# Kernel optimization log

Hardware: AMD Instinct MI355X
Metric: run time of the kernel (lower is better)

Reference implementation:

```python
import jax, jax.numpy as jnp
import numpy as np

# Dims: M=batch, T=time frames, B=bottleneck channels, H=intermediate channels, KK=kernel size
M, T, B, H, KK = 8, 4000, 128, 512, 3
DILATION = 2
EPS = 1e-8  # gLN eps (ConvTasNet convention)


def prelu(x, a):
    return jnp.where(x >= 0, x, a * x)


def gln(x, gamma, beta):
    # global layer norm over (time, channel) per sample; x: [M, T, C]
    m = jnp.mean(x, axis=(1, 2), keepdims=True)
    v = jnp.mean((x - m) ** 2, axis=(1, 2), keepdims=True)
    return gamma * (x - m) / jnp.sqrt(v + EPS) + beta


def depthwise_conv_same_reflect(x, w):
    # x: [M, C, L], w: [C, K]; dilation 1, 'same' padding with reflect mode
    K = w.shape[1]
    pl = (K - 1) // 2
    xp = jnp.pad(x, ((0, 0), (0, 0), (pl, K - 1 - pl)), mode='reflect')
    return jax.lax.conv_general_dilated(
        xp, w[:, None, :], (1,), 'VALID',
        feature_group_count=x.shape[1], dimension_numbers=('NCH', 'OIH', 'NCH'))


def setup_inputs() -> dict:
    key = jax.random.key(0)
    ks = jax.random.split(key, 12)
    f32 = jnp.float32
    return {
        'x': jax.random.normal(ks[0], (M, T, B), f32),
        'conv1_w': jax.random.normal(ks[1], (H, B), f32) * 0.05,
        'prelu1_a': jnp.asarray(0.25, f32),
        'norm1_g': jnp.ones((H,), f32),
        'norm1_b': jnp.zeros((H,), f32),
        'off_dw_w': jax.random.normal(ks[2], (H, KK), f32) * 0.02,
        'odc_prelu_a': jnp.asarray(0.25, f32),
        'off_pw_w': jax.random.normal(ks[3], (KK, H), f32) * 0.02,
        'opc_prelu_a': jnp.asarray(0.25, f32),
        'dw_w': jax.random.normal(ks[4], (H, KK), f32) * 0.05,
        'dw_b': jax.random.normal(ks[5], (H,), f32) * 0.01,
        'prelu2_a': jnp.asarray(0.25, f32),
        'norm2_g': jnp.ones((H,), f32),
        'norm2_b': jnp.zeros((H,), f32),
        'pw_w': jax.random.normal(ks[6], (B, H), f32) * 0.05,
    }


def reference(x, conv1_w, prelu1_a, norm1_g, norm1_b,
              off_dw_w, odc_prelu_a, off_pw_w, opc_prelu_a,
              dw_w, dw_b, prelu2_a, norm2_g, norm2_b, pw_w):
    dtype = x.dtype
    residual = x
    # 1x1 bottleneck conv -> PReLU -> gLN
    h = jnp.einsum('mtb,hb->mth', x, conv1_w)
    h = gln(prelu(h, prelu1_a), norm1_g, norm1_b)
    hc = jnp.moveaxis(h, 1, 2)  # [M, H, T]

    # --- offset prediction branch (PackedDeformConv1d) ---
    off = depthwise_conv_same_reflect(hc, off_dw_w)          # [M, H, T]
    off = prelu(off, odc_prelu_a)
    off = jnp.einsum('mct,kc->mkt', off, off_pw_w)           # [M, KK, T]
    off = prelu(off, opc_prelu_a)
    offsets = jnp.moveaxis(off, 1, 2)                        # [M, T, KK]

    # --- deformable depthwise conv (same padding, reflect) ---
    pad_tot = DILATION * (KK - 1)
    pl = pad_tot // 2
    xp = jnp.pad(hc, ((0, 0), (0, 0), (pl, pad_tot - pl)), mode='reflect')  # [M,H,Lp]
    Lp = T + pad_tot
    dil_pos = (jnp.arange(KK) * DILATION).astype(dtype)      # [KK]: 0, d, 2d
    t0 = jnp.arange(T, dtype=dtype)[:, None]                 # [T,1]
    Tpos = t0 + dil_pos[None, :] + offsets                   # [M,T,KK]
    Tpos = jnp.clip(Tpos, t0, t0 + dil_pos[-1])              # constrain to receptive field
    U = jnp.clip(jnp.floor(Tpos).astype(jnp.int32), 0, Lp - 2)
    Uf = U.astype(dtype)
    g0 = jax.nn.relu(1.0 - jnp.abs(Uf - Tpos))               # [M,T,KK]
    g1 = jax.nn.relu(1.0 - jnp.abs(Uf + 1.0 - Tpos))
    idx = jnp.broadcast_to(U.reshape(M, 1, T * KK), (M, H, T * KK))
    s0 = jnp.take_along_axis(xp, idx, axis=2).reshape(M, H, T, KK)
    s1 = jnp.take_along_axis(xp, idx + 1, axis=2).reshape(M, H, T, KK)
    sampled = g0[:, None] * s0 + g1[:, None] * s1            # [M,H,T,KK]
    y = jnp.einsum('mhtk,hk->mht', sampled, dw_w) + dw_b[None, :, None]

    # PReLU -> gLN -> 1x1 conv back to B channels, residual add
    y = jnp.moveaxis(y, 1, 2)                                # [M,T,H]
    y = gln(prelu(y, prelu2_a), norm2_g, norm2_b)
    out = jnp.einsum('mth,bh->mtb', y, pw_w)
    return out + residual
```

## Files before the change

kernel.cpp:

```cpp
#include <hip/hip_runtime.h>

#define Mdim 8
#define Tdim 4000
#define Bdim 128
#define Hdim 512
#define NPER (Tdim*Hdim)
#define EPSG 1e-8f

typedef __attribute__((ext_vector_type(8))) short short8;
typedef __attribute__((ext_vector_type(4))) float floatx4;

static __device__ __forceinline__ float bits2f(unsigned short s) {
  union { unsigned int u; float f; } v; v.u = ((unsigned int)s) << 16; return v.f;
}
static __device__ __forceinline__ unsigned short f2bits(float f) {
  union { float f; unsigned int u; } v; v.f = f;
  unsigned int u = v.u;
  u += 0x7fffu + ((u >> 16) & 1u);
  return (unsigned short)(u >> 16);
}
static __device__ __forceinline__ short8 pack8(const float4& a, const float4& b) {
  short8 v;
  v[0]=(short)f2bits(a.x); v[1]=(short)f2bits(a.y); v[2]=(short)f2bits(a.z); v[3]=(short)f2bits(a.w);
  v[4]=(short)f2bits(b.x); v[5]=(short)f2bits(b.y); v[6]=(short)f2bits(b.z); v[7]=(short)f2bits(b.w);
  return v;
}

__global__ __launch_bounds__(256) void k_conv1(
    const float* __restrict__ x,
    const float* __restrict__ w1,
    const float* __restrict__ a1p,
    unsigned short* __restrict__ Hbuf,
    float2* __restrict__ part1)
{
  __shared__ __align__(16) unsigned short ldsW[64*136];
  __shared__ __align__(16) unsigned short ltile[64*72];
  __shared__ float red[512];

  const int tid = threadIdx.x;
  const int t0 = blockIdx.x * 64;
  const int hh = blockIdx.y;
  const int m  = blockIdx.z;

  const int lane = tid & 63, wv = tid >> 6, quad = lane >> 4, l16 = lane & 15;
  int tr = t0 + wv*16 + l16;
  int trc = tr < Tdim ? tr : Tdim-1;
  const float* xrow = x + ((size_t)m*Tdim + trc)*Bdim;
  short8 afr[4];
  #pragma unroll
  for (int ks = 0; ks < 4; ++ks) {
    float4 fa = *(const float4*)&xrow[ks*32 + quad*8];
    float4 fb = *(const float4*)&xrow[ks*32 + quad*8 + 4];
    afr[ks] = pack8(fa, fb);
  }

  const float a1 = a1p[0];
  float lsum = 0.f, lss = 0.f;

  for (int hc = 0; hc < 4; ++hc) {
    const int h0 = (hh*4 + hc) * 64;
    __syncthreads();
    #pragma unroll
    for (int it = 0; it < 4; ++it) {
      int idx = (it*256 + tid) * 8;
      int r = idx >> 7, c = idx & 127;
      float4 fa = *(const float4*)&w1[(size_t)(h0 + r)*Bdim + c];
      float4 fb = *(const float4*)&w1[(size_t)(h0 + r)*Bdim + c + 4];
      *(short8*)&ldsW[r*136 + c] = pack8(fa, fb);
    }
    __syncthreads();

    floatx4 acc[4] = {};
    #pragma unroll
    for (int ks = 0; ks < 4; ++ks) {
      #pragma unroll
      for (int nt = 0; nt < 4; ++nt) {
        short8 bfr = *(const short8*)&ldsW[(nt*16 + l16)*136 + ks*32 + quad*8];
        acc[nt] = __builtin_amdgcn_mfma_f32_16x16x32_bf16(afr[ks], bfr, acc[nt], 0, 0, 0);
      }
    }

    #pragma unroll
    for (int nt = 0; nt < 4; ++nt) {
      int hl = nt*16 + l16;
      #pragma unroll
      for (int r = 0; r < 4; ++r) {
        int tl = wv*16 + quad*4 + r;
        float v = acc[nt][r];
        v = v >= 0.f ? v : a1 * v;
        if (t0 + tl < Tdim) { lsum += v; lss += v*v; }
        ltile[tl*72 + hl] = f2bits(v);
      }
    }
    __syncthreads();
    {
      int tr2 = tid >> 2, ck = (tid & 3) * 16;
      int tg = t0 + tr2;
      if (tg < Tdim) {
        unsigned short* dst = &Hbuf[((size_t)m*Tdim + tg)*Hdim + h0 + ck];
        *(short8*)&dst[0] = *(const short8*)&ltile[tr2*72 + ck];
        *(short8*)&dst[8] = *(const short8*)&ltile[tr2*72 + ck + 8];
      }
    }
  }

  red[tid] = lsum; red[256 + tid] = lss;
  __syncthreads();
  for (int s = 128; s > 0; s >>= 1) {
    if (tid < s) { red[tid] += red[tid + s]; red[256+tid] += red[256+tid+s]; }
    __syncthreads();
  }
  if (tid == 0)
    part1[((size_t)m*2 + hh)*63 + blockIdx.x] = make_float2(red[0], red[256]);
}

__global__ __launch_bounds__(256) void k_deform(
    const unsigned short* __restrict__ Hbuf,
    const float2* __restrict__ part1,
    const float* __restrict__ g1w,
    const float* __restrict__ b1w,
    const float* __restrict__ odw,
    const float* __restrict__ aodcp,
    const float* __restrict__ opw,
    const float* __restrict__ aopcp,
    const float* __restrict__ dww,
    const float* __restrict__ dwb,
    const float* __restrict__ a2p,
    unsigned short* __restrict__ Ybuf,
    float2* __restrict__ part2)
{
  __shared__ float s_stats[2];
  __shared__ float rsum[4], rss[4];
  const int tid = threadIdx.x, lane = tid & 63, w = tid >> 6;
  const int tb = blockIdx.x*8 + w*2;
  const int m = blockIdx.y;
  const int c8 = lane*8;
  const unsigned short* base = Hbuf + (size_t)m*Tdim*Hdim;

  short8 hrow[2][3];
  #pragma unroll
  for (int tt = 0; tt < 2; ++tt) {
    int t = tb + tt;
    int tm1 = (t == 0) ? 1 : t-1;
    int tp1 = (t == Tdim-1) ? Tdim-2 : t+1;
    hrow[tt][0] = *(const short8*)&base[(size_t)tm1*Hdim + c8];
    hrow[tt][1] = *(const short8*)&base[(size_t)t  *Hdim + c8];
    hrow[tt][2] = *(const short8*)&base[(size_t)tp1*Hdim + c8];
  }
  float g1v[8], b1v[8];
  #pragma unroll
  for (int j = 0; j < 8; j += 4) {
    *(float4*)&g1v[j] = *(const float4*)&g1w[c8 + j];
    *(float4*)&b1v[j] = *(const float4*)&b1w[c8 + j];
  }

  if (tid < 64) {
    float s = 0.f, q = 0.f;
    for (int i = lane; i < 126; i += 64) {
      float2 p = part1[(size_t)m*126 + i];
      s += p.x; q += p.y;
    }
    #pragma unroll
    for (int st = 32; st > 0; st >>= 1) { s += __shfl_xor(s, st); q += __shfl_xor(q, st); }
    if (lane == 0) { s_stats[0] = s; s_stats[1] = q; }
  }
  __syncthreads();
  const float invn = 1.0f/(float)NPER;
  const float mean1 = s_stats[0]*invn;
  const float var1  = fmaxf(s_stats[1]*invn - mean1*mean1, 0.f);
  const float inv1  = 1.0f/sqrtf(var1 + EPSG);

  float oa[2][3] = {};
  {
    const float aodc = aodcp[0];
    float wod[24], q0v[8], q1v[8], q2v[8];
    #pragma unroll
    for (int j = 0; j < 8; j += 4) {
      *(float4*)&q0v[j] = *(const float4*)&opw[c8 + j];
      *(float4*)&q1v[j] = *(const float4*)&opw[Hdim + c8 + j];
      *(float4*)&q2v[j] = *(const float4*)&opw[2*Hdim + c8 + j];
    }
    #pragma unroll
    for (int j = 0; j < 24; j += 4)
      *(float4*)&wod[j] = *(const float4*)&odw[c8*3 + j];

    #pragma unroll
    for (int j = 0; j < 8; ++j) {
      float A = g1v[j] * inv1;
      float C = b1v[j] - mean1*A;
      #pragma unroll
      for (int tt = 0; tt < 2; ++tt) {
        float fm = fmaf(A, bits2f((unsigned short)hrow[tt][0][j]), C);
        float fz = fmaf(A, bits2f((unsigned short)hrow[tt][1][j]), C);
        float fp = fmaf(A, bits2f((unsigned short)hrow[tt][2][j]), C);
        float d = fm*wod[j*3+0] + fz*wod[j*3+1] + fp*wod[j*3+2];
        d = d >= 0.f ? d : aodc*d;
        oa[tt][0] = fmaf(d, q0v[j], oa[tt][0]);
        oa[tt][1] = fmaf(d, q1v[j], oa[tt][1]);
        oa[tt][2] = fmaf(d, q2v[j], oa[tt][2]);
      }
    }
    #pragma unroll
    for (int s = 32; s > 0; s >>= 1) {
      #pragma unroll
      for (int tt = 0; tt < 2; ++tt) {
        oa[tt][0] += __shfl_xor(oa[tt][0], s);
        oa[tt][1] += __shfl_xor(oa[tt][1], s);
        oa[tt][2] += __shfl_xor(oa[tt][2], s);
      }
    }
  }

  const float aopc = aopcp[0];
  const float a2   = a2p[0];
  int I0[2][3], I1[2][3]; float G0[2][3], G1[2][3], GS[2][3];
  #pragma unroll
  for (int tt = 0; tt < 2; ++tt) {
    const float tf = (float)(tb + tt);
    #pragma unroll
    for (int k = 0; k < 3; ++k) {
      float off = oa[tt][k];
      off = off >= 0.f ? off : aopc*off;
      float pos = tf + (float)(2*k) + off;
      pos = fminf(fmaxf(pos, tf), tf + 4.0f);
      int U = (int)floorf(pos);
      if (U > Tdim + 2) U = Tdim + 2;
      float Uf = (float)U;
      G0[tt][k] = fmaxf(0.f, 1.f - fabsf(Uf - pos));
      G1[tt][k] = fmaxf(0.f, 1.f - fabsf(Uf + 1.f - pos));
      GS[tt][k] = G0[tt][k] + G1[tt][k];
      int ia = U - 2; ia = ia < 0 ? -ia : ia; if (ia > Tdim-1) ia = 2*(Tdim-1) - ia;
      int ib = U - 1; ib = ib < 0 ? -ib : ib; if (ib > Tdim-1) ib = 2*(Tdim-1) - ib;
      I0[tt][k] = ia; I1[tt][k] = ib;
    }
  }

  short8 s0v[2][3], s1v[2][3];
  #pragma unroll
  for (int tt = 0; tt < 2; ++tt)
    #pragma unroll
    for (int k = 0; k < 3; ++k) {
      s0v[tt][k] = *(const short8*)&base[(size_t)I0[tt][k]*Hdim + c8];
      s1v[tt][k] = *(const short8*)&base[(size_t)I1[tt][k]*Hdim + c8];
    }

  float bv[8], wd[24];
  #pragma unroll
  for (int j = 0; j < 8; j += 4)
    *(float4*)&bv[j] = *(const float4*)&dwb[c8 + j];
  #pragma unroll
  for (int j = 0; j < 24; j += 4)
    *(float4*)&wd[j] = *(const float4*)&dww[c8*3 + j];

  float lsum = 0.f, lss = 0.f;
  short8 yv[2];
  #pragma unroll
  for (int j = 0; j < 8; ++j) {
    float A = g1v[j] * inv1;
    float C = b1v[j] - mean1*A;
    float w0 = wd[j*3+0], w1 = wd[j*3+1], w2 = wd[j*3+2];
    #pragma unroll
    for (int tt = 0; tt < 2; ++tt) {
      float ybase = fmaf(C, w0*GS[tt][0] + w1*GS[tt][1] + w2*GS[tt][2], bv[j]);
      float t0s = fmaf(G1[tt][0], bits2f((unsigned short)s1v[tt][0][j]), G0[tt][0]*bits2f((unsigned short)s0v[tt][0][j]));
      float t1s = fmaf(G1[tt][1], bits2f((unsigned short)s1v[tt][1][j]), G0[tt][1]*bits2f((unsigned short)s0v[tt][1][j]));
      float t2s = fmaf(G1[tt][2], bits2f((unsigned short)s1v[tt][2][j]), G0[tt][2]*bits2f((unsigned short)s0v[tt][2][j]));
      float acc = w0*t0s + w1*t1s + w2*t2s;
      float y = fmaf(A, acc, ybase);
      float p = y >= 0.f ? y : a2*y;
      lsum += p; lss += p*p;
      yv[tt][j] = (short)f2bits(p);
    }
  }
  #pragma unroll
  for (int tt = 0; tt < 2; ++tt)
    *(short8*)&Ybuf[((size_t)m*Tdim + tb + tt)*Hdim + c8] = yv[tt];

  #pragma unroll
  for (int s = 32; s > 0; s >>= 1) {
    lsum += __shfl_xor(lsum, s);
    lss  += __shfl_xor(lss, s);
  }
  if (lane == 0) { rsum[w] = lsum; rss[w] = lss; }
  __syncthreads();
  if (tid == 0)
    part2[(size_t)m*500 + blockIdx.x] =
      make_float2(rsum[0]+rsum[1]+rsum[2]+rsum[3], rss[0]+rss[1]+rss[2]+rss[3]);
}

__global__ __launch_bounds__(64) void k_w2(
    const float2* __restrict__ part2,
    const float* __restrict__ g2w,
    const float* __restrict__ b2w,
    const float* __restrict__ pww,
    unsigned short* __restrict__ W2,
    float* __restrict__ const2)
{
  const int bid = blockIdx.x;
  const int m = bid >> 7, b = bid & 127;
  const int tid = threadIdx.x;

  float s = 0.f, q = 0.f;
  for (int i = tid; i < 500; i += 64) {
    float2 p = part2[(size_t)m*500 + i];
    s += p.x; q += p.y;
  }
  #pragma unroll
  for (int st = 32; st > 0; st >>= 1) { s += __shfl_xor(s, st); q += __shfl_xor(q, st); }

  const float invn = 1.0f/(float)NPER;
  const float mean2 = s*invn;
  const float var2  = fmaxf(q*invn - mean2*mean2, 0.f);
  const float inv2  = 1.0f/sqrtf(var2 + EPSG);

  const int j8 = tid*8;
  float g2v[8], b2v[8], pv[8];
  #pragma unroll
  for (int j = 0; j < 8; j += 4) {
    *(float4*)&g2v[j] = *(const float4*)&g2w[j8 + j];
    *(float4*)&b2v[j] = *(const float4*)&b2w[j8 + j];
    *(float4*)&pv[j]  = *(const float4*)&pww[(size_t)b*Hdim + j8 + j];
  }
  float csum = 0.f;
  short8 wv8;
  #pragma unroll
  for (int j = 0; j < 8; ++j) {
    float A = g2v[j] * inv2;
    float C = b2v[j] - mean2*A;
    csum = fmaf(C, pv[j], csum);
    wv8[j] = (short)f2bits(A*pv[j]);
  }
  *(short8*)&W2[((size_t)m*Bdim + b)*Hdim + j8] = wv8;

  #pragma unroll
  for (int st = 32; st > 0; st >>= 1) csum += __shfl_down(csum, st);
  if (tid == 0) const2[m*Bdim + b] = csum;
}

__global__ __launch_bounds__(256) void k_out(
    const unsigned short* __restrict__ Ybuf,
    const unsigned short* __restrict__ W2,
    const float* __restrict__ const2,
    const float* __restrict__ x,
    float* __restrict__ out)
{
  __shared__ __align__(16) unsigned short ldsW[64*136];
  __shared__ __align__(16) float ltf[64*68];
  const int tid = threadIdx.x;
  const int t0 = blockIdx.x*64;
  const int n0 = blockIdx.y*64;
  const int m  = blockIdx.z;
  const int lane = tid & 63, wv = tid >> 6, quad = lane >> 4, l16 = lane & 15;
  int tr = t0 + wv*16 + l16;
  int trc = tr < Tdim ? tr : Tdim-1;
  const unsigned short* arow = Ybuf + ((size_t)m*Tdim + trc)*Hdim;
  floatx4 acc[4] = {};
  for (int kc = 0; kc < 4; ++kc) {
    __syncthreads();
    #pragma unroll
    for (int it = 0; it < 4; ++it) {
      int idx = (it*256 + tid)*8;
      int r = idx >> 7, c = idx & 127;
      *(short8*)&ldsW[r*136 + c] =
        *(const short8*)&W2[((size_t)m*Bdim + n0 + r)*Hdim + kc*128 + c];
    }
    __syncthreads();
    #pragma unroll
    for (int ks = 0; ks < 4; ++ks) {
      short8 afr = *(const short8*)&arow[kc*128 + ks*32 + quad*8];
      #pragma unroll
      for (int nt = 0; nt < 4; ++nt) {
        short8 bfr = *(const short8*)&ldsW[(nt*16 + l16)*136 + ks*32 + quad*8];
        acc[nt] = __builtin_amdgcn_mfma_f32_16x16x32_bf16(afr, bfr, acc[nt], 0, 0, 0);
      }
    }
  }
  __syncthreads();
  #pragma unroll
  for (int nt = 0; nt < 4; ++nt) {
    int bl = nt*16 + l16;
    float cb = const2[m*Bdim + n0 + bl];
    #pragma unroll
    for (int r = 0; r < 4; ++r) {
      int tl = wv*16 + quad*4 + r;
      ltf[tl*68 + bl] = acc[nt][r] + cb;
    }
  }
  __syncthreads();
  {
    int tr2 = tid >> 2, ck = (tid & 3) * 16;
    int tg = t0 + tr2;
    if (tg < Tdim) {
      const float* xr = &x[((size_t)m*Tdim + tg)*Bdim + n0 + ck];
      float* orow = &out[((size_t)m*Tdim + tg)*Bdim + n0 + ck];
      #pragma unroll
      for (int j = 0; j < 4; ++j) {
        float4 v = *(const float4*)&ltf[tr2*68 + ck + j*4];
        float4 rx = *(const float4*)&xr[j*4];
        v.x += rx.x; v.y += rx.y; v.z += rx.z; v.w += rx.w;
        *(float4*)&orow[j*4] = v;
      }
    }
  }
}

extern "C" void kernel_launch(void* const* d_in, const int* in_sizes, int n_in,
                              void* d_out, int out_size, void* d_ws, size_t ws_size,
                              hipStream_t stream)
{
  (void)in_sizes; (void)n_in; (void)out_size; (void)ws_size;
  const float* x    = (const float*)d_in[0];
  const float* w1   = (const float*)d_in[1];
  const float* a1   = (const float*)d_in[2];
  const float* g1   = (const float*)d_in[3];
  const float* b1   = (const float*)d_in[4];
  const float* odw  = (const float*)d_in[5];
  const float* aodc = (const float*)d_in[6];
  const float* opw  = (const float*)d_in[7];
  const float* aopc = (const float*)d_in[8];
  const float* dww  = (const float*)d_in[9];
  const float* dwb  = (const float*)d_in[10];
  const float* a2   = (const float*)d_in[11];
  const float* g2   = (const float*)d_in[12];
  const float* b2   = (const float*)d_in[13];
  const float* pww  = (const float*)d_in[14];
  float* out = (float*)d_out;

  char* ws = (char*)d_ws;
  const size_t OFF_P1 = 0;
  const size_t OFF_C2 = 8192;
  const size_t OFF_P2 = 12288;
  const size_t OFF_W2 = 44288;
  const size_t OFF_H  = 1092864;
  const size_t OFF_Y  = 33860864;
  float2* part1  = (float2*)(ws + OFF_P1);
  float*  const2 = (float*)(ws + OFF_C2);
  float2* part2  = (float2*)(ws + OFF_P2);
  unsigned short* W2   = (unsigned short*)(ws + OFF_W2);
  unsigned short* Hbuf = (unsigned short*)(ws + OFF_H);
  unsigned short* Ybuf = (unsigned short*)(ws + OFF_Y);

  k_conv1 <<<dim3(63, 2, 8), 256, 0, stream>>>(x, w1, a1, Hbuf, part1);
  k_deform<<<dim3(500, 8), 256, 0, stream>>>(Hbuf, part1, g1, b1, odw, aodc, opw, aopc, dww, dwb, a2, Ybuf, part2);
  k_w2    <<<dim3(1024), 64, 0, stream>>>(part2, g2, b2, pww, W2, const2);
  k_out   <<<dim3(63, 2, 8), 256, 0, stream>>>(Ybuf, W2, const2, x, out);
}
```

Before: 165.6 us.

## Stage H time tile in LDS for deform gather and pre-swizzle GEMM weights

```diff
diff --git a/kernel.cpp b/kernel.cpp
--- a/kernel.cpp
+++ b/kernel.cpp
@@ -6,6 +6,7 @@
 #define Hdim 512
 #define NPER (Tdim*Hdim)
 #define EPSG 1e-8f
+#define ROWS 69
 
 typedef __attribute__((ext_vector_type(8))) short short8;
 typedef __attribute__((ext_vector_type(4))) float floatx4;
@@ -26,22 +27,38 @@
   return v;
 }
 
+#define LDS_FENCE() do { \
+  asm volatile("s_waitcnt lgkmcnt(0)" ::: "memory"); \
+  __builtin_amdgcn_sched_barrier(0); \
+} while (0)
+
+__global__ __launch_bounds__(256) void k_prep(
+    const float* __restrict__ w1, unsigned short* __restrict__ w1r)
+{
+  int i = blockIdx.x*256 + threadIdx.x;
+  int lane = i & 63, f = i >> 6;
+  int nt = f & 3, ks = (f >> 2) & 3, hc = f >> 4;
+  int h = hc*64 + nt*16 + (lane & 15);
+  int c = ks*32 + (lane >> 4)*8;
+  const float* src = &w1[(size_t)h*Bdim + c];
+  float4 a = *(const float4*)src;
+  float4 b = *(const float4*)(src + 4);
+  *(short8*)&w1r[(size_t)i*8] = pack8(a, b);
+}
+
 __global__ __launch_bounds__(256) void k_conv1(
     const float* __restrict__ x,
-    const float* __restrict__ w1,
+    const unsigned short* __restrict__ w1r,
     const float* __restrict__ a1p,
     unsigned short* __restrict__ Hbuf,
     float2* __restrict__ part1)
 {
-  __shared__ __align__(16) unsigned short ldsW[64*136];
   __shared__ __align__(16) unsigned short ltile[64*72];
   __shared__ float red[512];
 
   const int tid = threadIdx.x;
   const int t0 = blockIdx.x * 64;
-  const int hh = blockIdx.y;
-  const int m  = blockIdx.z;
-
+  const int m  = blockIdx.y;
   const int lane = tid & 63, wv = tid >> 6, quad = lane >> 4, l16 = lane & 15;
   int tr = t0 + wv*16 + l16;
   int trc = tr < Tdim ? tr : Tdim-1;
@@ -55,30 +72,17 @@
   }
 
   const float a1 = a1p[0];
+  const short8* wf = (const short8*)w1r + lane;
   float lsum = 0.f, lss = 0.f;
 
-  for (int hc = 0; hc < 4; ++hc) {
-    const int h0 = (hh*4 + hc) * 64;
-    __syncthreads();
-    #pragma unroll
-    for (int it = 0; it < 4; ++it) {
-      int idx = (it*256 + tid) * 8;
-      int r = idx >> 7, c = idx & 127;
-      float4 fa = *(const float4*)&w1[(size_t)(h0 + r)*Bdim + c];
-      float4 fb = *(const float4*)&w1[(size_t)(h0 + r)*Bdim + c + 4];
-      *(short8*)&ldsW[r*136 + c] = pack8(fa, fb);
-    }
-    __syncthreads();
-
+  for (int hc = 0; hc < 8; ++hc) {
     floatx4 acc[4] = {};
     #pragma unroll
-    for (int ks = 0; ks < 4; ++ks) {
-      #pragma unroll
-      for (int nt = 0; nt < 4; ++nt) {
-        short8 bfr = *(const short8*)&ldsW[(nt*16 + l16)*136 + ks*32 + quad*8];
-        acc[nt] = __builtin_amdgcn_mfma_f32_16x16x32_bf16(afr[ks], bfr, acc[nt], 0, 0, 0);
-      }
-    }
+    for (int ks = 0; ks < 4; ++ks)
+      #pragma unroll
+      for (int nt = 0; nt < 4; ++nt)
+        acc[nt] = __builtin_amdgcn_mfma_f32_16x16x32_bf16(
+            afr[ks], wf[(hc*16 + ks*4 + nt)*64], acc[nt], 0, 0, 0);
 
     #pragma unroll
     for (int nt = 0; nt < 4; ++nt) {
@@ -92,16 +96,17 @@
         ltile[tl*72 + hl] = f2bits(v);
       }
     }
-    __syncthreads();
+    LDS_FENCE();
     {
       int tr2 = tid >> 2, ck = (tid & 3) * 16;
       int tg = t0 + tr2;
       if (tg < Tdim) {
-        unsigned short* dst = &Hbuf[((size_t)m*Tdim + tg)*Hdim + h0 + ck];
+        unsigned short* dst = &Hbuf[((size_t)m*Tdim + tg)*Hdim + hc*64 + ck];
         *(short8*)&dst[0] = *(const short8*)&ltile[tr2*72 + ck];
         *(short8*)&dst[8] = *(const short8*)&ltile[tr2*72 + ck + 8];
       }
     }
+    LDS_FENCE();
   }
 
   red[tid] = lsum; red[256 + tid] = lss;
@@ -111,7 +116,7 @@
     __syncthreads();
   }
   if (tid == 0)
-    part1[((size_t)m*2 + hh)*63 + blockIdx.x] = make_float2(red[0], red[256]);
+    part1[(size_t)m*63 + blockIdx.x] = make_float2(red[0], red[256]);
 }
 
 __global__ __launch_bounds__(256) void k_deform(
@@ -129,65 +134,88 @@
     unsigned short* __restrict__ Ybuf,
     float2* __restrict__ part2)
 {
+  __shared__ __align__(16) unsigned short tile[ROWS*512];
   __shared__ float s_stats[2];
   __shared__ float rsum[4], rss[4];
   const int tid = threadIdx.x, lane = tid & 63, w = tid >> 6;
-  const int tb = blockIdx.x*8 + w*2;
+  const int t0 = blockIdx.x * 64;
   const int m = blockIdx.y;
   const int c8 = lane*8;
   const unsigned short* base = Hbuf + (size_t)m*Tdim*Hdim;
 
-  short8 hrow[2][3];
-  #pragma unroll
-  for (int tt = 0; tt < 2; ++tt) {
-    int t = tb + tt;
-    int tm1 = (t == 0) ? 1 : t-1;
-    int tp1 = (t == Tdim-1) ? Tdim-2 : t+1;
-    hrow[tt][0] = *(const short8*)&base[(size_t)tm1*Hdim + c8];
-    hrow[tt][1] = *(const short8*)&base[(size_t)t  *Hdim + c8];
-    hrow[tt][2] = *(const short8*)&base[(size_t)tp1*Hdim + c8];
-  }
-  float g1v[8], b1v[8];
-  #pragma unroll
-  for (int j = 0; j < 8; j += 4) {
-    *(float4*)&g1v[j] = *(const float4*)&g1w[c8 + j];
-    *(float4*)&b1v[j] = *(const float4*)&b1w[c8 + j];
+  short8 stg[17];
+  #pragma unroll
+  for (int i = 0; i < 17; ++i) {
+    int s = t0 - 2 + w + i*4;
+    s = s < 0 ? -s : s;
+    if (s > Tdim-1) s = 2*(Tdim-1) - s;
+    stg[i] = *(const short8*)&base[(size_t)s*Hdim + c8];
+  }
+  short8 extra;
+  if (w == 0) {
+    int s = t0 + 66;
+    if (s > Tdim-1) s = 2*(Tdim-1) - s;
+    extra = *(const short8*)&base[(size_t)s*Hdim + c8];
   }
 
   if (tid < 64) {
     float s = 0.f, q = 0.f;
-    for (int i = lane; i < 126; i += 64) {
-      float2 p = part1[(size_t)m*126 + i];
-      s += p.x; q += p.y;
-    }
+    if (lane < 63) { float2 p = part1[(size_t)m*63 + lane]; s = p.x; q = p.y; }
     #pragma unroll
     for (int st = 32; st > 0; st >>= 1) { s += __shfl_xor(s, st); q += __shfl_xor(q, st); }
     if (lane == 0) { s_stats[0] = s; s_stats[1] = q; }
   }
+
+  #pragma unroll
+  for (int i = 0; i < 17; ++i)
+    *(short8*)&tile[(w + i*4)*512 + c8] = stg[i];
+  if (w == 0) *(short8*)&tile[68*512 + c8] = extra;
+
   __syncthreads();
+
   const float invn = 1.0f/(float)NPER;
   const float mean1 = s_stats[0]*invn;
   const float var1  = fmaxf(s_stats[1]*invn - mean1*mean1, 0.f);
   const float inv1  = 1.0f/sqrtf(var1 + EPSG);
 
-  float oa[2][3] = {};
-  {
-    const float aodc = aodcp[0];
-    float wod[24], q0v[8], q1v[8], q2v[8];
-    #pragma unroll
-    for (int j = 0; j < 8; j += 4) {
-      *(float4*)&q0v[j] = *(const float4*)&opw[c8 + j];
-      *(float4*)&q1v[j] = *(const float4*)&opw[Hdim + c8 + j];
-      *(float4*)&q2v[j] = *(const float4*)&opw[2*Hdim + c8 + j];
-    }
-    #pragma unroll
-    for (int j = 0; j < 24; j += 4)
-      *(float4*)&wod[j] = *(const float4*)&odw[c8*3 + j];
-
+  const float aodc = aodcp[0], aopc = aopcp[0], a2 = a2p[0];
+  float wod[24], q0v[8], q1v[8], q2v[8], wd[24], bv[8], Ax[8], Cx[8];
+  #pragma unroll
+  for (int j = 0; j < 8; j += 4) {
+    *(float4*)&q0v[j] = *(const float4*)&opw[c8 + j];
+    *(float4*)&q1v[j] = *(const float4*)&opw[Hdim + c8 + j];
+    *(float4*)&q2v[j] = *(const float4*)&opw[2*Hdim + c8 + j];
+    *(float4*)&bv[j]  = *(const float4*)&dwb[c8 + j];
+  }
+  #pragma unroll
+  for (int j = 0; j < 24; j += 4) {
+    *(float4*)&wod[j] = *(const float4*)&odw[c8*3 + j];
+    *(float4*)&wd[j]  = *(const float4*)&dww[c8*3 + j];
+  }
+  #pragma unroll
+  for (int j = 0; j < 8; ++j) {
+    Ax[j] = g1w[c8 + j] * inv1;
+    Cx[j] = b1w[c8 + j] - mean1*Ax[j];
+  }
+
+  float lsum = 0.f, lss = 0.f;
+  #pragma unroll 1
+  for (int it = 0; it < 16; it += 2) {
+    const int t = t0 + w*16 + it;
+    if (t >= Tdim) break;
+    const int sb = t - t0 + 2;
+
+    short8 hrow[2][3];
+    #pragma unroll
+    for (int tt = 0; tt < 2; ++tt)
+      #pragma unroll
+      for (int k = 0; k < 3; ++k)
+        hrow[tt][k] = *(const short8*)&tile[(sb + tt - 1 + k)*512 + c8];
+
+    float oa[2][3] = {};
     #pragma unroll
     for (int j = 0; j < 8; ++j) {
-      float A = g1v[j] * inv1;
-      float C = b1v[j] - mean1*A;
+      float A = Ax[j], C = Cx[j];
       #pragma unroll
       for (int tt = 0; tt < 2; ++tt) {
         float fm = fmaf(A, bits2f((unsigned short)hrow[tt][0][j]), C);
@@ -201,90 +229,77 @@
       }
     }
     #pragma unroll
-    for (int s = 32; s > 0; s >>= 1) {
+    for (int st = 32; st > 0; st >>= 1) {
       #pragma unroll
       for (int tt = 0; tt < 2; ++tt) {
-        oa[tt][0] += __shfl_xor(oa[tt][0], s);
-        oa[tt][1] += __shfl_xor(oa[tt][1], s);
-        oa[tt][2] += __shfl_xor(oa[tt][2], s);
-      }
-    }
-  }
-
-  const float aopc = aopcp[0];
-  const float a2   = a2p[0];
-  int I0[2][3], I1[2][3]; float G0[2][3], G1[2][3], GS[2][3];
-  #pragma unroll
-  for (int tt = 0; tt < 2; ++tt) {
-    const float tf = (float)(tb + tt);
-    #pragma unroll
-    for (int k = 0; k < 3; ++k) {
-      float off = oa[tt][k];
-      off = off >= 0.f ? off : aopc*off;
-      float pos = tf + (float)(2*k) + off;
-      pos = fminf(fmaxf(pos, tf), tf + 4.0f);
-      int U = (int)floorf(pos);
-      if (U > Tdim + 2) U = Tdim + 2;
-      float Uf = (float)U;
-      G0[tt][k] = fmaxf(0.f, 1.f - fabsf(Uf - pos));
-      G1[tt][k] = fmaxf(0.f, 1.f - fabsf(Uf + 1.f - pos));
-      GS[tt][k] = G0[tt][k] + G1[tt][k];
-      int ia = U - 2; ia = ia < 0 ? -ia : ia; if (ia > Tdim-1) ia = 2*(Tdim-1) - ia;
-      int ib = U - 1; ib = ib < 0 ? -ib : ib; if (ib > Tdim-1) ib = 2*(Tdim-1) - ib;
-      I0[tt][k] = ia; I1[tt][k] = ib;
-    }
-  }
-
-  short8 s0v[2][3], s1v[2][3];
-  #pragma unroll
-  for (int tt = 0; tt < 2; ++tt)
-    #pragma unroll
-    for (int k = 0; k < 3; ++k) {
-      s0v[tt][k] = *(const short8*)&base[(size_t)I0[tt][k]*Hdim + c8];
-      s1v[tt][k] = *(const short8*)&base[(size_t)I1[tt][k]*Hdim + c8];
-    }
-
-  float bv[8], wd[24];
-  #pragma unroll
-  for (int j = 0; j < 8; j += 4)
-    *(float4*)&bv[j] = *(const float4*)&dwb[c8 + j];
-  #pragma unroll
-  for (int j = 0; j < 24; j += 4)
-    *(float4*)&wd[j] = *(const float4*)&dww[c8*3 + j];
-
-  float lsum = 0.f, lss = 0.f;
-  short8 yv[2];
-  #pragma unroll
-  for (int j = 0; j < 8; ++j) {
-    float A = g1v[j] * inv1;
-    float C = b1v[j] - mean1*A;
-    float w0 = wd[j*3+0], w1 = wd[j*3+1], w2 = wd[j*3+2];
+        oa[tt][0] += __shfl_xor(oa[tt][0], st);
+        oa[tt][1] += __shfl_xor(oa[tt][1], st);
+        oa[tt][2] += __shfl_xor(oa[tt][2], st);
+      }
+    }
+
+    int S0[2][3], S1[2][3]; float G0[2][3], G1[2][3], GS[2][3];
     #pragma unroll
     for (int tt = 0; tt < 2; ++tt) {
-      float ybase = fmaf(C, w0*GS[tt][0] + w1*GS[tt][1] + w2*GS[tt][2], bv[j]);
-      float t0s = fmaf(G1[tt][0], bits2f((unsigned short)s1v[tt][0][j]), G0[tt][0]*bits2f((unsigned short)s0v[tt][0][j]));
-      float t1s = fmaf(G1[tt][1], bits2f((unsigned short)s1v[tt][1][j]), G0[tt][1]*bits2f((unsigned short)s0v[tt][1][j]));
-      float t2s = fmaf(G1[tt][2], bits2f((unsigned short)s1v[tt][2][j]), G0[tt][2]*bits2f((unsigned short)s0v[tt][2][j]));
-      float acc = w0*t0s + w1*t1s + w2*t2s;
-      float y = fmaf(A, acc, ybase);
-      float p = y >= 0.f ? y : a2*y;
-      lsum += p; lss += p*p;
-      yv[tt][j] = (short)f2bits(p);
-    }
-  }
-  #pragma unroll
-  for (int tt = 0; tt < 2; ++tt)
-    *(short8*)&Ybuf[((size_t)m*Tdim + tb + tt)*Hdim + c8] = yv[tt];
-
-  #pragma unroll
-  for (int s = 32; s > 0; s >>= 1) {
-    lsum += __shfl_xor(lsum, s);
-    lss  += __shfl_xor(lss, s);
+      const float tf = (float)(t + tt);
+      #pragma unroll
+      for (int k = 0; k < 3; ++k) {
+        float off = oa[tt][k];
+        off = off >= 0.f ? off : aopc*off;
+        float pos = tf + (float)(2*k) + off;
+        pos = fminf(fmaxf(pos, tf), tf + 4.0f);
+        int U = (int)floorf(pos);
+        if (U > Tdim + 2) U = Tdim + 2;
+        float Uf = (float)U;
+        G0[tt][k] = fmaxf(0.f, 1.f - fabsf(Uf - pos));
+        G1[tt][k] = fmaxf(0.f, 1.f - fabsf(Uf + 1.f - pos));
+        GS[tt][k] = G0[tt][k] + G1[tt][k];
+        S0[tt][k] = U - t0;
+        S1[tt][k] = U - t0 + 1;
+      }
+    }
+
+    short8 s0v[2][3], s1v[2][3];
+    #pragma unroll
+    for (int tt = 0; tt < 2; ++tt)
+      #pragma unroll
+      for (int k = 0; k < 3; ++k) {
+        s0v[tt][k] = *(const short8*)&tile[S0[tt][k]*512 + c8];
+        s1v[tt][k] = *(const short8*)&tile[S1[tt][k]*512 + c8];
+      }
+
+    short8 yv[2];
+    #pragma unroll
+    for (int j = 0; j < 8; ++j) {
+      float A = Ax[j], C = Cx[j];
+      float w0 = wd[j*3+0], w1 = wd[j*3+1], w2 = wd[j*3+2];
+      #pragma unroll
+      for (int tt = 0; tt < 2; ++tt) {
+        float ybase = fmaf(C, w0*GS[tt][0] + w1*GS[tt][1] + w2*GS[tt][2], bv[j]);
+        float t0s = fmaf(G1[tt][0], bits2f((unsigned short)s1v[tt][0][j]), G0[tt][0]*bits2f((unsigned short)s0v[tt][0][j]));
+        float t1s = fmaf(G1[tt][1], bits2f((unsigned short)s1v[tt][1][j]), G0[tt][1]*bits2f((unsigned short)s0v[tt][1][j]));
+        float t2s = fmaf(G1[tt][2], bits2f((unsigned short)s1v[tt][2][j]), G0[tt][2]*bits2f((unsigned short)s0v[tt][2][j]));
+        float acc2 = w0*t0s + w1*t1s + w2*t2s;
+        float y = fmaf(A, acc2, ybase);
+        float p = y >= 0.f ? y : a2*y;
+        lsum += p; lss += p*p;
+        yv[tt][j] = (short)f2bits(p);
+      }
+    }
+    #pragma unroll
+    for (int tt = 0; tt < 2; ++tt)
+      *(short8*)&Ybuf[((size_t)m*Tdim + t + tt)*Hdim + c8] = yv[tt];
+  }
+
+  #pragma unroll
+  for (int st = 32; st > 0; st >>= 1) {
+    lsum += __shfl_xor(lsum, st);
+    lss  += __shfl_xor(lss, st);
   }
   if (lane == 0) { rsum[w] = lsum; rss[w] = lss; }
   __syncthreads();
   if (tid == 0)
-    part2[(size_t)m*500 + blockIdx.x] =
+    part2[(size_t)m*63 + blockIdx.x] =
       make_float2(rsum[0]+rsum[1]+rsum[2]+rsum[3], rss[0]+rss[1]+rss[2]+rss[3]);
 }
 
@@ -293,7 +308,7 @@
     const float* __restrict__ g2w,
     const float* __restrict__ b2w,
     const float* __restrict__ pww,
-    unsigned short* __restrict__ W2,
+    unsigned short* __restrict__ W2r,
     float* __restrict__ const2)
 {
   const int bid = blockIdx.x;
@@ -301,10 +316,7 @@
   const int tid = threadIdx.x;
 
   float s = 0.f, q = 0.f;
-  for (int i = tid; i < 500; i += 64) {
-    float2 p = part2[(size_t)m*500 + i];
-    s += p.x; q += p.y;
-  }
+  if (tid < 63) { float2 p = part2[(size_t)m*63 + tid]; s = p.x; q = p.y; }
   #pragma unroll
   for (int st = 32; st > 0; st >>= 1) { s += __shfl_xor(s, st); q += __shfl_xor(q, st); }
 
@@ -330,7 +342,13 @@
     csum = fmaf(C, pv[j], csum);
     wv8[j] = (short)f2bits(A*pv[j]);
   }
-  *(short8*)&W2[((size_t)m*Bdim + b)*Hdim + j8] = wv8;
+  {
+    int half = b >> 6, nt = (b >> 4) & 3, l16 = b & 15;
+    int kc = tid >> 4, ks = (tid >> 2) & 3, quad = tid & 3;
+    int lane = quad*16 + l16;
+    size_t f = ((((size_t)(m*2 + half)*4 + kc)*4 + ks)*4 + nt);
+    *(short8*)&W2r[(f*64 + lane)*8] = wv8;
+  }
 
   #pragma unroll
   for (int st = 32; st > 0; st >>= 1) csum += __shfl_down(csum, st);
@@ -339,43 +357,35 @@
 
 __global__ __launch_bounds__(256) void k_out(
     const unsigned short* __restrict__ Ybuf,
-    const unsigned short* __restrict__ W2,
+    const unsigned short* __restrict__ W2r,
     const float* __restrict__ const2,
     const float* __restrict__ x,
     float* __restrict__ out)
 {
-  __shared__ __align__(16) unsigned short ldsW[64*136];
   __shared__ __align__(16) float ltf[64*68];
   const int tid = threadIdx.x;
   const int t0 = blockIdx.x*64;
-  const int n0 = blockIdx.y*64;
+  const int half = blockIdx.y;
+  const int n0 = half*64;
   const int m  = blockIdx.z;
   const int lane = tid & 63, wv = tid >> 6, quad = lane >> 4, l16 = lane & 15;
   int tr = t0 + wv*16 + l16;
   int trc = tr < Tdim ? tr : Tdim-1;
   const unsigned short* arow = Ybuf + ((size_t)m*Tdim + trc)*Hdim;
+  const short8* wf = (const short8*)W2r + (size_t)(m*2 + half)*64*64 + lane;
+
   floatx4 acc[4] = {};
-  for (int kc = 0; kc < 4; ++kc) {
-    __syncthreads();
-    #pragma unroll
-    for (int it = 0; it < 4; ++it) {
-      int idx = (it*256 + tid)*8;
-      int r = idx >> 7, c = idx & 127;
-      *(short8*)&ldsW[r*136 + c] =
-        *(const short8*)&W2[((size_t)m*Bdim + n0 + r)*Hdim + kc*128 + c];
-    }
-    __syncthreads();
+  #pragma unroll
+  for (int kc = 0; kc < 4; ++kc)
     #pragma unroll
     for (int ks = 0; ks < 4; ++ks) {
       short8 afr = *(const short8*)&arow[kc*128 + ks*32 + quad*8];
       #pragma unroll
-      for (int nt = 0; nt < 4; ++nt) {
-        short8 bfr = *(const short8*)&ldsW[(nt*16 + l16)*136 + ks*32 + quad*8];
-        acc[nt] = __builtin_amdgcn_mfma_f32_16x16x32_bf16(afr, bfr, acc[nt], 0, 0, 0);
-      }
-    }
-  }
-  __syncthreads();
+      for (int nt = 0; nt < 4; ++nt)
+        acc[nt] = __builtin_amdgcn_mfma_f32_16x16x32_bf16(
+            afr, wf[((kc*4 + ks)*4 + nt)*64], acc[nt], 0, 0, 0);
+    }
+
   #pragma unroll
   for (int nt = 0; nt < 4; ++nt) {
     int bl = nt*16 + l16;
@@ -386,7 +396,7 @@
       ltf[tl*68 + bl] = acc[nt][r] + cb;
     }
   }
-  __syncthreads();
+  LDS_FENCE();
   {
     int tr2 = tid >> 2, ck = (tid & 3) * 16;
     int tg = t0 + tr2;
@@ -427,21 +437,24 @@
   float* out = (float*)d_out;
 
   char* ws = (char*)d_ws;
-  const size_t OFF_P1 = 0;
-  const size_t OFF_C2 = 8192;
-  const size_t OFF_P2 = 12288;
-  const size_t OFF_W2 = 44288;
-  const size_t OFF_H  = 1092864;
-  const size_t OFF_Y  = 33860864;
+  const size_t OFF_P1  = 0;
+  const size_t OFF_C2  = 4096;
+  const size_t OFF_P2  = 8192;
+  const size_t OFF_W1R = 12288;
+  const size_t OFF_W2  = 143360;
+  const size_t OFF_H   = 1191936;
+  const size_t OFF_Y   = 33959936;
   float2* part1  = (float2*)(ws + OFF_P1);
   float*  const2 = (float*)(ws + OFF_C2);
   float2* part2  = (float2*)(ws + OFF_P2);
-  unsigned short* W2   = (unsigned short*)(ws + OFF_W2);
+  unsigned short* w1r  = (unsigned short*)(ws + OFF_W1R);
+  unsigned short* W2r  = (unsigned short*)(ws + OFF_W2);
   unsigned short* Hbuf = (unsigned short*)(ws + OFF_H);
   unsigned short* Ybuf = (unsigned short*)(ws + OFF_Y);
 
-  k_conv1 <<<dim3(63, 2, 8), 256, 0, stream>>>(x, w1, a1, Hbuf, part1);
-  k_deform<<<dim3(500, 8), 256, 0, stream>>>(Hbuf, part1, g1, b1, odw, aodc, opw, aopc, dww, dwb, a2, Ybuf, part2);
-  k_w2    <<<dim3(1024), 64, 0, stream>>>(part2, g2, b2, pww, W2, const2);
-  k_out   <<<dim3(63, 2, 8), 256, 0, stream>>>(Ybuf, W2, const2, x, out);
-}
+  k_prep  <<<dim3(32), 256, 0, stream>>>(w1, w1r);
+  k_conv1 <<<dim3(63, 8), 256, 0, stream>>>(x, w1r, a1, Hbuf, part1);
+  k_deform<<<dim3(63, 8), 256, 0, stream>>>(Hbuf, part1, g1, b1, odw, aodc, opw, aopc, dww, dwb, a2, Ybuf, part2);
+  k_w2    <<<dim3(1024), 64, 0, stream>>>(part2, g2, b2, pww, W2r, const2);
+  k_out   <<<dim3(63, 2, 8), 256, 0, stream>>>(Ybuf, W2r, const2, x, out);
+}
```

After: 169.9 us. 2.6% more time.

## Fuse four kernels into one cooperative persistent kernel with grid syncs

Applied to the files above, without the earlier changes.

```diff
diff --git a/kernel.cpp b/kernel.cpp
--- a/kernel.cpp
+++ b/kernel.cpp
@@ -1,4 +1,5 @@
 #include <hip/hip_runtime.h>
+#include <hip/hip_cooperative_groups.h>
 
 #define Mdim 8
 #define Tdim 4000
@@ -26,26 +27,36 @@
   return v;
 }
 
-__global__ __launch_bounds__(256) void k_conv1(
-    const float* __restrict__ x,
-    const float* __restrict__ w1,
-    const float* __restrict__ a1p,
-    unsigned short* __restrict__ Hbuf,
-    float2* __restrict__ part1)
-{
-  __shared__ __align__(16) unsigned short ldsW[64*136];
-  __shared__ __align__(16) unsigned short ltile[64*72];
-  __shared__ float red[512];
+#define LDS_FENCE() do { \
+  asm volatile("s_waitcnt lgkmcnt(0)" ::: "memory"); \
+  __builtin_amdgcn_sched_barrier(0); \
+} while (0)
+
+struct P {
+  const float *x, *w1, *a1, *g1, *b1, *odw, *aodc, *opw, *aopc, *dww, *dwb, *a2, *g2, *b2, *pww;
+  float2 *part1, *part2;
+  float *const2;
+  unsigned short *W2r, *Hbuf, *Ybuf;
+  float *out;
+};
+
+#define SMEM_BYTES 28672
+
+__device__ __forceinline__ void phase_conv1(const P& p, int task, char* smem) {
+  unsigned short* ldsW  = (unsigned short*)smem;
+  unsigned short* ltile = (unsigned short*)(smem + 17408);
+  float* red = (float*)(smem + 26624);
 
   const int tid = threadIdx.x;
-  const int t0 = blockIdx.x * 64;
-  const int hh = blockIdx.y;
-  const int m  = blockIdx.z;
-
+  const int tile = task % 63;
+  const int rem  = task / 63;
+  const int hh = rem & 1;
+  const int m  = rem >> 1;
+  const int t0 = tile * 64;
   const int lane = tid & 63, wv = tid >> 6, quad = lane >> 4, l16 = lane & 15;
   int tr = t0 + wv*16 + l16;
   int trc = tr < Tdim ? tr : Tdim-1;
-  const float* xrow = x + ((size_t)m*Tdim + trc)*Bdim;
+  const float* xrow = p.x + ((size_t)m*Tdim + trc)*Bdim;
   short8 afr[4];
   #pragma unroll
   for (int ks = 0; ks < 4; ++ks) {
@@ -53,8 +64,7 @@
     float4 fb = *(const float4*)&xrow[ks*32 + quad*8 + 4];
     afr[ks] = pack8(fa, fb);
   }
-
-  const float a1 = a1p[0];
+  const float a1 = p.a1[0];
   float lsum = 0.f, lss = 0.f;
 
   for (int hc = 0; hc < 4; ++hc) {
@@ -64,8 +74,8 @@
     for (int it = 0; it < 4; ++it) {
       int idx = (it*256 + tid) * 8;
       int r = idx >> 7, c = idx & 127;
-      float4 fa = *(const float4*)&w1[(size_t)(h0 + r)*Bdim + c];
-      float4 fb = *(const float4*)&w1[(size_t)(h0 + r)*Bdim + c + 4];
+      float4 fa = *(const float4*)&p.w1[(size_t)(h0 + r)*Bdim + c];
+      float4 fb = *(const float4*)&p.w1[(size_t)(h0 + r)*Bdim + c + 4];
       *(short8*)&ldsW[r*136 + c] = pack8(fa, fb);
     }
     __syncthreads();
@@ -97,7 +107,7 @@
       int tr2 = tid >> 2, ck = (tid & 3) * 16;
       int tg = t0 + tr2;
       if (tg < Tdim) {
-        unsigned short* dst = &Hbuf[((size_t)m*Tdim + tg)*Hdim + h0 + ck];
+        unsigned short* dst = &p.Hbuf[((size_t)m*Tdim + tg)*Hdim + h0 + ck];
         *(short8*)&dst[0] = *(const short8*)&ltile[tr2*72 + ck];
         *(short8*)&dst[8] = *(const short8*)&ltile[tr2*72 + ck + 8];
       }
@@ -111,31 +121,22 @@
     __syncthreads();
   }
   if (tid == 0)
-    part1[((size_t)m*2 + hh)*63 + blockIdx.x] = make_float2(red[0], red[256]);
-}
-
-__global__ __launch_bounds__(256) void k_deform(
-    const unsigned short* __restrict__ Hbuf,
-    const float2* __restrict__ part1,
-    const float* __restrict__ g1w,
-    const float* __restrict__ b1w,
-    const float* __restrict__ odw,
-    const float* __restrict__ aodcp,
-    const float* __restrict__ opw,
-    const float* __restrict__ aopcp,
-    const float* __restrict__ dww,
-    const float* __restrict__ dwb,
-    const float* __restrict__ a2p,
-    unsigned short* __restrict__ Ybuf,
-    float2* __restrict__ part2)
-{
-  __shared__ float s_stats[2];
-  __shared__ float rsum[4], rss[4];
+    p.part1[((size_t)m*2 + hh)*63 + tile] = make_float2(red[0], red[256]);
+  __syncthreads();
+}
+
+__device__ __forceinline__ void phase_deform(const P& p, int task, char* smem) {
+  float* s_stats = (float*)smem;
+  float* rsum = (float*)smem + 2;
+  float* rss  = (float*)smem + 6;
   const int tid = threadIdx.x, lane = tid & 63, w = tid >> 6;
-  const int tb = blockIdx.x*8 + w*2;
-  const int m = blockIdx.y;
+  const int tx = task % 500;
+  const int m  = task / 500;
+  const int tb = tx*8 + w*2;
   const int c8 = lane*8;
-  const unsigned short* base = Hbuf + (size_t)m*Tdim*Hdim;
+  const unsigned short* base = p.Hbuf + (size_t)m*Tdim*Hdim;
+
+  __syncthreads();
 
   short8 hrow[2][3];
   #pragma unroll
@@ -150,15 +151,15 @@
   float g1v[8], b1v[8];
   #pragma unroll
   for (int j = 0; j < 8; j += 4) {
-    *(float4*)&g1v[j] = *(const float4*)&g1w[c8 + j];
-    *(float4*)&b1v[j] = *(const float4*)&b1w[c8 + j];
+    *(float4*)&g1v[j] = *(const float4*)&p.g1[c8 + j];
+    *(float4*)&b1v[j] = *(const float4*)&p.b1[c8 + j];
   }
 
   if (tid < 64) {
     float s = 0.f, q = 0.f;
     for (int i = lane; i < 126; i += 64) {
-      float2 p = part1[(size_t)m*126 + i];
-      s += p.x; q += p.y;
+      float2 pp = p.part1[(size_t)m*126 + i];
+      s += pp.x; q += pp.y;
     }
     #pragma unroll
     for (int st = 32; st > 0; st >>= 1) { s += __shfl_xor(s, st); q += __shfl_xor(q, st); }
@@ -172,17 +173,17 @@
 
   float oa[2][3] = {};
   {
-    const float aodc = aodcp[0];
+    const float aodc = p.aodc[0];
     float wod[24], q0v[8], q1v[8], q2v[8];
     #pragma unroll
     for (int j = 0; j < 8; j += 4) {
-      *(float4*)&q0v[j] = *(const float4*)&opw[c8 + j];
-      *(float4*)&q1v[j] = *(const float4*)&opw[Hdim + c8 + j];
-      *(float4*)&q2v[j] = *(const float4*)&opw[2*Hdim + c8 + j];
+      *(float4*)&q0v[j] = *(const float4*)&p.opw[c8 + j];
+      *(float4*)&q1v[j] = *(const float4*)&p.opw[Hdim + c8 + j];
+      *(float4*)&q2v[j] = *(const float4*)&p.opw[2*Hdim + c8 + j];
     }
     #pragma unroll
     for (int j = 0; j < 24; j += 4)
-      *(float4*)&wod[j] = *(const float4*)&odw[c8*3 + j];
+      *(float4*)&wod[j] = *(const float4*)&p.odw[c8*3 + j];
 
     #pragma unroll
     for (int j = 0; j < 8; ++j) {
@@ -211,8 +212,8 @@
     }
   }
 
-  const float aopc = aopcp[0];
-  const float a2   = a2p[0];
+  const float aopc = p.aopc[0];
+  const float a2   = p.a2[0];
   int I0[2][3], I1[2][3]; float G0[2][3], G1[2][3], GS[2][3];
   #pragma unroll
   for (int tt = 0; tt < 2; ++tt) {
@@ -247,10 +248,10 @@
   float bv[8], wd[24];
   #pragma unroll
   for (int j = 0; j < 8; j += 4)
-    *(float4*)&bv[j] = *(const float4*)&dwb[c8 + j];
+    *(float4*)&bv[j] = *(const float4*)&p.dwb[c8 + j];
   #pragma unroll
   for (int j = 0; j < 24; j += 4)
-    *(float4*)&wd[j] = *(const float4*)&dww[c8*3 + j];
+    *(float4*)&wd[j] = *(const float4*)&p.dww[c8*3 + j];
 
   float lsum = 0.f, lss = 0.f;
   short8 yv[2];
@@ -267,14 +268,14 @@
       float t2s = fmaf(G1[tt][2], bits2f((unsigned short)s1v[tt][2][j]), G0[tt][2]*bits2f((unsigned short)s0v[tt][2][j]));
       float acc = w0*t0s + w1*t1s + w2*t2s;
       float y = fmaf(A, acc, ybase);
-      float p = y >= 0.f ? y : a2*y;
-      lsum += p; lss += p*p;
-      yv[tt][j] = (short)f2bits(p);
+      float pp = y >= 0.f ? y : a2*y;
+      lsum += pp; lss += pp*pp;
+      yv[tt][j] = (short)f2bits(pp);
     }
   }
   #pragma unroll
   for (int tt = 0; tt < 2; ++tt)
-    *(short8*)&Ybuf[((size_t)m*Tdim + tb + tt)*Hdim + c8] = yv[tt];
+    *(short8*)&p.Ybuf[((size_t)m*Tdim + tb + tt)*Hdim + c8] = yv[tt];
 
   #pragma unroll
   for (int s = 32; s > 0; s >>= 1) {
@@ -284,26 +285,19 @@
   if (lane == 0) { rsum[w] = lsum; rss[w] = lss; }
   __syncthreads();
   if (tid == 0)
-    part2[(size_t)m*500 + blockIdx.x] =
+    p.part2[(size_t)m*500 + tx] =
       make_float2(rsum[0]+rsum[1]+rsum[2]+rsum[3], rss[0]+rss[1]+rss[2]+rss[3]);
 }
 
-__global__ __launch_bounds__(64) void k_w2(
-    const float2* __restrict__ part2,
-    const float* __restrict__ g2w,
-    const float* __restrict__ b2w,
-    const float* __restrict__ pww,
-    unsigned short* __restrict__ W2,
-    float* __restrict__ const2)
-{
-  const int bid = blockIdx.x;
-  const int m = bid >> 7, b = bid & 127;
+__device__ __forceinline__ void phase_w2(const P& p, int task) {
   const int tid = threadIdx.x;
+  if (tid >= 64) return;
+  const int m = task >> 7, b = task & 127;
 
   float s = 0.f, q = 0.f;
   for (int i = tid; i < 500; i += 64) {
-    float2 p = part2[(size_t)m*500 + i];
-    s += p.x; q += p.y;
+    float2 pp = p.part2[(size_t)m*500 + i];
+    s += pp.x; q += pp.y;
   }
   #pragma unroll
   for (int st = 32; st > 0; st >>= 1) { s += __shfl_xor(s, st); q += __shfl_xor(q, st); }
@@ -317,9 +311,9 @@
   float g2v[8], b2v[8], pv[8];
   #pragma unroll
   for (int j = 0; j < 8; j += 4) {
-    *(float4*)&g2v[j] = *(const float4*)&g2w[j8 + j];
-    *(float4*)&b2v[j] = *(const float4*)&b2w[j8 + j];
-    *(float4*)&pv[j]  = *(const float4*)&pww[(size_t)b*Hdim + j8 + j];
+    *(float4*)&g2v[j] = *(const float4*)&p.g2[j8 + j];
+    *(float4*)&b2v[j] = *(const float4*)&p.b2[j8 + j];
+    *(float4*)&pv[j]  = *(const float4*)&p.pww[(size_t)b*Hdim + j8 + j];
   }
   float csum = 0.f;
   short8 wv8;
@@ -330,69 +324,63 @@
     csum = fmaf(C, pv[j], csum);
     wv8[j] = (short)f2bits(A*pv[j]);
   }
-  *(short8*)&W2[((size_t)m*Bdim + b)*Hdim + j8] = wv8;
+  {
+    int half = b >> 6, nt = (b >> 4) & 3, l16 = b & 15;
+    int kc = tid >> 4, ks = (tid >> 2) & 3, quad = tid & 3;
+    int lane = quad*16 + l16;
+    size_t f = ((((size_t)(m*2 + half)*4 + kc)*4 + ks)*4 + nt);
+    *(short8*)&p.W2r[(f*64 + lane)*8] = wv8;
+  }
 
   #pragma unroll
   for (int st = 32; st > 0; st >>= 1) csum += __shfl_down(csum, st);
-  if (tid == 0) const2[m*Bdim + b] = csum;
-}
-
-__global__ __launch_bounds__(256) void k_out(
-    const unsigned short* __restrict__ Ybuf,
-    const unsigned short* __restrict__ W2,
-    const float* __restrict__ const2,
-    const float* __restrict__ x,
-    float* __restrict__ out)
-{
-  __shared__ __align__(16) unsigned short ldsW[64*136];
-  __shared__ __align__(16) float ltf[64*68];
+  if (tid == 0) p.const2[m*Bdim + b] = csum;
+}
+
+__device__ __forceinline__ void phase_out(const P& p, int task, char* smem) {
+  float* ltf = (float*)smem;
   const int tid = threadIdx.x;
-  const int t0 = blockIdx.x*64;
-  const int n0 = blockIdx.y*64;
-  const int m  = blockIdx.z;
+  const int tile = task % 63;
+  const int rem = task / 63;
+  const int half = rem & 1;
+  const int m = rem >> 1;
+  const int t0 = tile*64;
+  const int n0 = half*64;
   const int lane = tid & 63, wv = tid >> 6, quad = lane >> 4, l16 = lane & 15;
   int tr = t0 + wv*16 + l16;
   int trc = tr < Tdim ? tr : Tdim-1;
-  const unsigned short* arow = Ybuf + ((size_t)m*Tdim + trc)*Hdim;
+  const unsigned short* arow = p.Ybuf + ((size_t)m*Tdim + trc)*Hdim;
+  const short8* wf = (const short8*)p.W2r + (size_t)(m*2 + half)*64*64 + lane;
+
   floatx4 acc[4] = {};
-  for (int kc = 0; kc < 4; ++kc) {
-    __syncthreads();
-    #pragma unroll
-    for (int it = 0; it < 4; ++it) {
-      int idx = (it*256 + tid)*8;
-      int r = idx >> 7, c = idx & 127;
-      *(short8*)&ldsW[r*136 + c] =
-        *(const short8*)&W2[((size_t)m*Bdim + n0 + r)*Hdim + kc*128 + c];
-    }
-    __syncthreads();
+  #pragma unroll
+  for (int kc = 0; kc < 4; ++kc)
     #pragma unroll
     for (int ks = 0; ks < 4; ++ks) {
       short8 afr = *(const short8*)&arow[kc*128 + ks*32 + quad*8];
       #pragma unroll
-      for (int nt = 0; nt < 4; ++nt) {
-        short8 bfr = *(const short8*)&ldsW[(nt*16 + l16)*136 + ks*32 + quad*8];
-        acc[nt] = __builtin_amdgcn_mfma_f32_16x16x32_bf16(afr, bfr, acc[nt], 0, 0, 0);
-      }
-    }
-  }
-  __syncthreads();
+      for (int nt = 0; nt < 4; ++nt)
+        acc[nt] = __builtin_amdgcn_mfma_f32_16x16x32_bf16(
+            afr, wf[((kc*4 + ks)*4 + nt)*64], acc[nt], 0, 0, 0);
+    }
+
   #pragma unroll
   for (int nt = 0; nt < 4; ++nt) {
     int bl = nt*16 + l16;
-    float cb = const2[m*Bdim + n0 + bl];
+    float cb = p.const2[m*Bdim + n0 + bl];
     #pragma unroll
     for (int r = 0; r < 4; ++r) {
       int tl = wv*16 + quad*4 + r;
       ltf[tl*68 + bl] = acc[nt][r] + cb;
     }
   }
-  __syncthreads();
+  LDS_FENCE();
   {
     int tr2 = tid >> 2, ck = (tid & 3) * 16;
     int tg = t0 + tr2;
     if (tg < Tdim) {
-      const float* xr = &x[((size_t)m*Tdim + tg)*Bdim + n0 + ck];
-      float* orow = &out[((size_t)m*Tdim + tg)*Bdim + n0 + ck];
+      const float* xr = &p.x[((size_t)m*Tdim + tg)*Bdim + n0 + ck];
+      float* orow = &p.out[((size_t)m*Tdim + tg)*Bdim + n0 + ck];
       #pragma unroll
       for (int j = 0; j < 4; ++j) {
         float4 v = *(const float4*)&ltf[tr2*68 + ck + j*4];
@@ -402,6 +390,39 @@
       }
     }
   }
+  LDS_FENCE();
+}
+
+__global__ __launch_bounds__(256, 4) void k_fused(P p) {
+  __shared__ __align__(16) char smem[SMEM_BYTES];
+  cooperative_groups::grid_group g = cooperative_groups::this_grid();
+
+  for (int t = blockIdx.x; t < 1008; t += gridDim.x) phase_conv1(p, t, smem);
+  __threadfence();
+  g.sync();
+  for (int t = blockIdx.x; t < 4000; t += gridDim.x) phase_deform(p, t, smem);
+  __threadfence();
+  g.sync();
+  for (int t = blockIdx.x; t < 1024; t += gridDim.x) phase_w2(p, t);
+  __threadfence();
+  g.sync();
+  for (int t = blockIdx.x; t < 1008; t += gridDim.x) phase_out(p, t, smem);
+}
+
+__global__ __launch_bounds__(256, 4) void k_p1(P p) {
+  __shared__ __align__(16) char smem[SMEM_BYTES];
+  phase_conv1(p, blockIdx.x, smem);
+}
+__global__ __launch_bounds__(256, 4) void k_p2(P p) {
+  __shared__ __align__(16) char smem[SMEM_BYTES];
+  phase_deform(p, blockIdx.x, smem);
+}
+__global__ __launch_bounds__(256, 4) void k_p3(P p) {
+  phase_w2(p, blockIdx.x);
+}
+__global__ __launch_bounds__(256, 4) void k_p4(P p) {
+  __shared__ __align__(16) char smem[SMEM_BYTES];
+  phase_out(p, blockIdx.x, smem);
 }
 
 extern "C" void kernel_launch(void* const* d_in, const int* in_sizes, int n_in,
@@ -409,39 +430,66 @@
                               hipStream_t stream)
 {
   (void)in_sizes; (void)n_in; (void)out_size; (void)ws_size;
-  const float* x    = (const float*)d_in[0];
-  const float* w1   = (const float*)d_in[1];
-  const float* a1   = (const float*)d_in[2];
-  const float* g1   = (const float*)d_in[3];
-  const float* b1   = (const float*)d_in[4];
-  const float* odw  = (const float*)d_in[5];
-  const float* aodc = (const float*)d_in[6];
-  const float* opw  = (const float*)d_in[7];
-  const float* aopc = (const float*)d_in[8];
-  const float* dww  = (const float*)d_in[9];
-  const float* dwb  = (const float*)d_in[10];
-  const float* a2   = (const float*)d_in[11];
-  const float* g2   = (const float*)d_in[12];
-  const float* b2   = (const float*)d_in[13];
-  const float* pww  = (const float*)d_in[14];
-  float* out = (float*)d_out;
 
   char* ws = (char*)d_ws;
   const size_t OFF_P1 = 0;
-  const size_t OFF_C2 = 8192;
-  const size_t OFF_P2 = 12288;
-  const size_t OFF_W2 = 44288;
-  const size_t OFF_H  = 1092864;
-  const size_t OFF_Y  = 33860864;
-  float2* part1  = (float2*)(ws + OFF_P1);
-  float*  const2 = (float*)(ws + OFF_C2);
-  float2* part2  = (float2*)(ws + OFF_P2);
-  unsigned short* W2   = (unsigned short*)(ws + OFF_W2);
-  unsigned short* Hbuf = (unsigned short*)(ws + OFF_H);
-  unsigned short* Ybuf = (unsigned short*)(ws + OFF_Y);
-
-  k_conv1 <<<dim3(63, 2, 8), 256, 0, stream>>>(x, w1, a1, Hbuf, part1);
-  k_deform<<<dim3(500, 8), 256, 0, stream>>>(Hbuf, part1, g1, b1, odw, aodc, opw, aopc, dww, dwb, a2, Ybuf, part2);
-  k_w2    <<<dim3(1024), 64, 0, stream>>>(part2, g2, b2, pww, W2, const2);
-  k_out   <<<dim3(63, 2, 8), 256, 0, stream>>>(Ybuf, W2, const2, x, out);
-}
+  const size_t OFF_P2 = 8192;
+  const size_t OFF_C2 = 40960;
+  const size_t OFF_W2 = 45056;
+  const size_t OFF_H  = 1093632;
+  const size_t OFF_Y  = 33861632;
+
+  P hp;
+  hp.x    = (const float*)d_in[0];
+  hp.w1   = (const float*)d_in[1];
+  hp.a1   = (const float*)d_in[2];
+  hp.g1   = (const float*)d_in[3];
+  hp.b1   = (const float*)d_in[4];
+  hp.odw  = (const float*)d_in[5];
+  hp.aodc = (const float*)d_in[6];
+  hp.opw  = (const float*)d_in[7];
+  hp.aopc = (const float*)d_in[8];
+  hp.dww  = (const float*)d_in[9];
+  hp.dwb  = (const float*)d_in[10];
+  hp.a2   = (const float*)d_in[11];
+  hp.g2   = (const float*)d_in[12];
+  hp.b2   = (const float*)d_in[13];
+  hp.pww  = (const float*)d_in[14];
+  hp.part1  = (float2*)(ws + OFF_P1);
+  hp.part2  = (float2*)(ws + OFF_P2);
+  hp.const2 = (float*)(ws + OFF_C2);
+  hp.W2r  = (unsigned short*)(ws + OFF_W2);
+  hp.Hbuf = (unsigned short*)(ws + OFF_H);
+  hp.Ybuf = (unsigned short*)(ws + OFF_Y);
+  hp.out  = (float*)d_out;
+
+  static int coopGrid = -2;
+  if (coopGrid == -2) {
+    int maxb = 0;
+    if (hipOccupancyMaxActiveBlocksPerMultiprocessor(&maxb, (const void*)k_fused, 256, 0)
+          == hipSuccess && maxb > 0) {
+      long g = (long)maxb * 256;
+      if (g > 1024) g = 1024;
+      coopGrid = (int)g;
+    } else {
+      coopGrid = -1;
+    }
+  }
+
+  bool launched = false;
+  if (coopGrid > 0) {
+    void* params[] = { (void*)&hp };
+    if (hipLaunchCooperativeKernel((const void*)k_fused, dim3(coopGrid), dim3(256),
+                                   params, 0, stream) == hipSuccess) {
+      launched = true;
+    } else {
+      coopGrid = -1;
+    }
+  }
+  if (!launched) {
+    k_p1<<<dim3(1008), 256, 0, stream>>>(hp);
+    k_p2<<<dim3(4000), 256, 0, stream>>>(hp);
+    k_p3<<<dim3(1024), 256, 0, stream>>>(hp);
+    k_p4<<<dim3(1008), 256, 0, stream>>>(hp);
+  }
+}
```

Measured after the change: 525.3 us. 3.17x slower.
